# Optimization experiments

Measured on AMD Instinct MI355X. Metric: run time of the kernel, lower is better.

The kernel has to match this reference:

```python
import jax, jax.numpy as jnp
import numpy as np

H = 768
R = 24


def setup_inputs() -> dict:
    key = jax.random.key(0)
    ks = jax.random.split(key, 9)
    B, S = 4, 256
    hidden = jax.random.normal(ks[0], (B, S, H), dtype=jnp.float32)
    # ConcatHandshaking fc: Linear(2H -> H); torch weight shape (out,in)=(H,2H)
    fc_w = jax.random.normal(ks[1], (H, 2 * H), dtype=jnp.float32) * (1.0 / np.sqrt(2 * H))
    fc_b = jnp.zeros((H,), dtype=jnp.float32)
    # h2t: Linear(H -> 2)
    h2t_w = jax.random.normal(ks[2], (2, H), dtype=jnp.float32) * (1.0 / np.sqrt(H))
    h2t_b = jnp.zeros((2,), dtype=jnp.float32)
    # h2h / t2t TaggingProjector: R independent Linear(H -> 3), batched as (R,3,H)
    h2h_w = jax.random.normal(ks[3], (R, 3, H), dtype=jnp.float32) * (1.0 / np.sqrt(H))
    h2h_b = jnp.zeros((R, 3), dtype=jnp.float32)
    t2t_w = jax.random.normal(ks[4], (R, 3, H), dtype=jnp.float32) * (1.0 / np.sqrt(H))
    t2t_b = jnp.zeros((R, 3), dtype=jnp.float32)
    return {
        "hidden": hidden,
        "fc_w": fc_w, "fc_b": fc_b,
        "h2t_w": h2t_w, "h2t_b": h2t_b,
        "h2h_w": h2h_w, "h2h_b": h2h_b,
        "t2t_w": t2t_w, "t2t_b": t2t_b,
    }


def _handshaking(hidden, fc_w, fc_b):
    # hidden: (B, S, H). Pairs (i, j) with i <= j in row-major (torch loop) order.
    S = hidden.shape[1]
    idx_i, idx_j = jnp.triu_indices(S)  # each (P,), P = S(S+1)/2
    # concat([h_i, h_j]) @ W^T == h_i @ Wl^T + h_j @ Wr^T  (avoids (B,P,2H) buffer)
    Wl = fc_w[:, :H]  # (H, H)
    Wr = fc_w[:, H:]  # (H, H)
    left = jnp.einsum('bsh,oh->bso', hidden, Wl)   # (B, S, H)
    right = jnp.einsum('bsh,oh->bso', hidden, Wr)  # (B, S, H)
    hs = jnp.tanh(left[:, idx_i, :] + right[:, idx_j, :] + fc_b)  # (B, P, H)
    return hs


def reference(hidden, fc_w, fc_b, h2t_w, h2t_b, h2h_w, h2h_b, t2t_w, t2t_b):
    hs = _handshaking(hidden, fc_w, fc_b)  # (B, P, H)
    # h2t: plain Linear(H->2), logits (no softmax in original)
    h2t = jnp.einsum('bph,oh->bpo', hs, h2t_w) + h2t_b  # (B, P, 2)
    # TaggingProjector: batched per-relation Linear(H->3), then softmax over tags
    h2h = jax.nn.softmax(jnp.einsum('bph,rth->brpt', hs, h2h_w) + h2h_b[None, :, None, :], axis=-1)
    t2t = jax.nn.softmax(jnp.einsum('bph,rth->brpt', hs, t2t_w) + t2t_b[None, :, None, :], axis=-1)
    return (h2t, h2h, t2t)
```

## Files before the change

### kernel.cpp

```cpp
#include <hip/hip_runtime.h>
#include <hip/hip_bf16.h>

#define H 768
#define SEQ 256
#define NPAIR 32896
#define NTOT 131584
#define NOUTP 160
#define OFF_H2H 263168u
#define OFF_T2T 9737216u

#define N_BPK 122880
#define SCL 2.8853900817779268f

#define CH 32
#define NCH 24
#define BSLOT 12288
#define SLAB_STR 166

typedef short bf16x8 __attribute__((ext_vector_type(8)));
typedef float f32x4 __attribute__((ext_vector_type(4)));

__device__ __forceinline__ float bf_lo(int w){ return __uint_as_float(((unsigned)w) << 16); }
__device__ __forceinline__ float bf_hi(int w){ return __uint_as_float(((unsigned)w) & 0xffff0000u); }
__device__ __forceinline__ float bfu(unsigned short u){ return __uint_as_float(((unsigned)u) << 16); }
__device__ __forceinline__ int cvtpk(float lo, float hi) {
    int r;
    asm("v_cvt_pk_bf16_f32 %0, %1, %2" : "=v"(r) : "v"(lo), "v"(hi));
    return r;
}
__device__ __forceinline__ unsigned short bf16r(float x){
    unsigned int u = __float_as_uint(x);
    u += 0x7fffu + ((u >> 16) & 1u);
    return (unsigned short)(u >> 16);
}
__device__ __forceinline__ float tanh_e(float el, float er) {
    float e = el * er;
    return fmaf(-2.0f, __builtin_amdgcn_rcpf(e + 1.0f), 1.0f);
}
__device__ __forceinline__ bf16x8 prod_frag(int4 lv, int4 rv) {
    int4 st;
    st.x = cvtpk(tanh_e(bf_lo(lv.x), bf_lo(rv.x)), tanh_e(bf_hi(lv.x), bf_hi(rv.x)));
    st.y = cvtpk(tanh_e(bf_lo(lv.y), bf_lo(rv.y)), tanh_e(bf_hi(lv.y), bf_hi(rv.y)));
    st.z = cvtpk(tanh_e(bf_lo(lv.z), bf_lo(rv.z)), tanh_e(bf_hi(lv.z), bf_hi(rv.z)));
    st.w = cvtpk(tanh_e(bf_lo(lv.w), bf_lo(rv.w)), tanh_e(bf_hi(lv.w), bf_hi(rv.w)));
    return __builtin_bit_cast(bf16x8, st);
}

typedef const __attribute__((address_space(1))) unsigned int* as1_u32p;
typedef __attribute__((address_space(3))) unsigned int* as3_u32p;
__device__ __forceinline__ void gload_lds16(const void* g, void* l) {
    __builtin_amdgcn_global_load_lds((as1_u32p)g, (as3_u32p)l, 16, 0, 0);
}

__device__ __forceinline__ int row_start(int i) { return i * SEQ - (i * (i - 1)) / 2; }
__device__ __forceinline__ void pair_ij(int p, int& oi, int& oj) {
    double disc = 263169.0 - 8.0 * (double)p;
    int i = (int)((513.0 - sqrt(disc)) * 0.5);
    if (i > 0 && row_start(i) > p) --i;
    while (row_start(i + 1) <= p) ++i;
    oi = i;
    oj = i + (p - row_start(i));
}
__device__ __forceinline__ int batch_of(int g) {
    return (g >= 3 * NPAIR) ? 3 : (g >= 2 * NPAIR) ? 2 : (g >= NPAIR) ? 1 : 0;
}

__global__ __launch_bounds__(256) void pack_kernel(
    const float* __restrict__ h2t_w, const float* __restrict__ h2h_w,
    const float* __restrict__ t2t_w, const float* __restrict__ h2t_b,
    const float* __restrict__ h2h_b, const float* __restrict__ t2t_b,
    unsigned short* __restrict__ Bpk, float* __restrict__ bc)
{
    int idx = blockIdx.x * 256 + threadIdx.x;
    if (idx < N_BPK) {
        int j = idx & 7, lane = (idx >> 3) & 63, rest = idx >> 9;
        int f = rest % 10, c = rest / 10;
        int n = f * 16 + (lane & 15);
        int k = c * CH + ((lane >> 4) << 3) + j;
        float v = 0.f;
        if (n < 2)        v = h2t_w[n * H + k];
        else if (n < 74)  v = h2h_w[(n - 2) * H + k];
        else if (n < 146) v = t2t_w[(n - 74) * H + k];
        Bpk[c * 6144 + (idx - c * 5120)] = bf16r(v);
    } else if (idx < N_BPK + NOUTP) {
        int q = idx - N_BPK;
        float v = 0.f;
        if (q < 2)        v = h2t_b[q];
        else if (q < 74)  v = h2h_b[q - 2];
        else if (q < 146) v = t2t_b[q - 74];
        bc[q] = v;
    }
}

__global__ __launch_bounds__(256, 2) void lr_mfma(
    const float* __restrict__ hidden, const float* __restrict__ fc_w,
    const float* __restrict__ fc_b,
    unsigned short* __restrict__ LB, unsigned short* __restrict__ RB)
{
    __shared__ __align__(16) char sm[16384];
    const int tid = threadIdx.x, l = tid & 63, w = tid >> 6;
    const int wm = w >> 1, wn = w & 1;
    const int m0 = blockIdx.x * 64, n0 = blockIdx.y * 64;
    f32x4 acc[2][2] = {};
    for (int c = 0; c < 12; ++c) {
        const int k0 = c * 64;
        #pragma unroll
        for (int it = 0; it < 2; ++it) {
            int idx = tid + it * 256;
            int row = idx >> 3, k8 = idx & 7;
            const float4* src = reinterpret_cast<const float4*>(hidden + (size_t)(m0 + row) * H + k0 + k8 * 8);
            float4 a = src[0], bq = src[1];
            int4 st;
            st.x = cvtpk(a.x, a.y);  st.y = cvtpk(a.z, a.w);
            st.z = cvtpk(bq.x, bq.y); st.w = cvtpk(bq.z, bq.w);
            *reinterpret_cast<int4*>(sm + row * 128 + ((k8 * 16) ^ ((row & 7) << 4))) = st;
        }
        #pragma unroll
        for (int it = 0; it < 2; ++it) {
            int idx = tid + it * 256;
            int row = idx >> 3, k8 = idx & 7;
            const float* fsrc = (n0 < H)
                ? fc_w + (size_t)(n0 + row) * (2 * H) + k0 + k8 * 8
                : fc_w + (size_t)(n0 - H + row) * (2 * H) + H + k0 + k8 * 8;
            const float4* src = reinterpret_cast<const float4*>(fsrc);
            float4 a = src[0], bq = src[1];
            int4 st;
            st.x = cvtpk(a.x, a.y);  st.y = cvtpk(a.z, a.w);
            st.z = cvtpk(bq.x, bq.y); st.w = cvtpk(bq.z, bq.w);
            *reinterpret_cast<int4*>(sm + 8192 + row * 128 + ((k8 * 16) ^ ((row & 7) << 4))) = st;
        }
        __syncthreads();
        #pragma unroll
        for (int kk = 0; kk < 2; ++kk) {
            const int sl = kk * 4 + (l >> 4);
            const int swz = (l & 7) << 4;
            bf16x8 af[2], bfr[2];
            #pragma unroll
            for (int a = 0; a < 2; ++a) {
                int row = 32 * wm + 16 * a + (l & 15);
                af[a] = *reinterpret_cast<const bf16x8*>(sm + row * 128 + ((sl * 16) ^ swz));
            }
            #pragma unroll
            for (int f = 0; f < 2; ++f) {
                int row = 32 * wn + 16 * f + (l & 15);
                bfr[f] = *reinterpret_cast<const bf16x8*>(sm + 8192 + row * 128 + ((sl * 16) ^ swz));
            }
            #pragma unroll
            for (int a = 0; a < 2; ++a)
                #pragma unroll
                for (int f = 0; f < 2; ++f)
                    acc[a][f] = __builtin_amdgcn_mfma_f32_16x16x32_bf16(af[a], bfr[f], acc[a][f], 0, 0, 0);
        }
        __syncthreads();
    }
    #pragma unroll
    for (int a = 0; a < 2; ++a)
        #pragma unroll
        for (int f = 0; f < 2; ++f)
            #pragma unroll
            for (int r = 0; r < 4; ++r) {
                int row = m0 + 32 * wm + 16 * a + 4 * (l >> 4) + r;
                int col = n0 + 32 * wn + 16 * f + (l & 15);
                float v = acc[a][f][r];
                if (n0 < H) LB[(size_t)row * H + col] =
                    bf16r(__builtin_amdgcn_exp2f((v + fc_b[col]) * SCL));
                else        RB[(size_t)row * H + (col - H)] =
                    bf16r(__builtin_amdgcn_exp2f(v * SCL));
            }
}

__global__ __launch_bounds__(256, 4) void pair_mfma(
    const unsigned short* __restrict__ LB, const unsigned short* __restrict__ RB,
    const unsigned short* __restrict__ Bpk, const float* __restrict__ bc,
    float* __restrict__ out)
{
    __shared__ __align__(16) char sm[25216];
    int*   iOf  = reinterpret_cast<int*>(sm);
    int*   jOf  = reinterpret_cast<int*>(sm + 256);
    float* bc_s = reinterpret_cast<float*>(sm + 24576);

    const int tid = threadIdx.x, l = tid & 63, w = tid >> 6;
    const int g0 = blockIdx.x * 64;
    const int b = batch_of(g0);
    const int p0 = g0 - b * NPAIR;

    if (tid < 64) {
        int i, j; pair_ij(p0 + tid, i, j);
        iOf[tid] = (b * SEQ + i) * H;
        jOf[tid] = (b * SEQ + j) * H;
    }
    if (tid < NOUTP) bc_s[tid] = bc[tid];
    __syncthreads();

    const int row = 16 * w + (l & 15);
    const unsigned short* lp = LB + iOf[row] + ((l >> 4) << 3);
    const unsigned short* rp = RB + jOf[row] + ((l >> 4) << 3);
    __syncthreads();

    const char* bp = reinterpret_cast<const char*>(Bpk) + w * 1024 + l * 16;
    const int d0 = w * 1024;

    f32x4 acc[10] = {};
    int4 lv[3], rv[3];

    {
        gload_lds16(bp,        sm + d0);
        gload_lds16(bp + 4096, sm + 4096 + d0);
        gload_lds16(bp + 8192, sm + 8192 + d0);
        __builtin_amdgcn_sched_barrier(0);
    }
    lv[0] = *reinterpret_cast<const int4*>(lp);
    rv[0] = *reinterpret_cast<const int4*>(rp);
    lv[1] = *reinterpret_cast<const int4*>(lp + CH);
    rv[1] = *reinterpret_cast<const int4*>(rp + CH);
    asm volatile("s_waitcnt vmcnt(4)" ::: "memory");
    __builtin_amdgcn_s_barrier();
    __builtin_amdgcn_sched_barrier(0);

    #pragma unroll
    for (int c = 0; c < NCH - 2; ++c) {
        char* bufn = sm + (((c + 1) & 1) ? BSLOT : 0);
        const char* bn = bp + (c + 1) * BSLOT;
        gload_lds16(bn,        bufn + d0);
        gload_lds16(bn + 4096, bufn + 4096 + d0);
        gload_lds16(bn + 8192, bufn + 8192 + d0);
        __builtin_amdgcn_sched_barrier(0);
        bf16x8 a0 = prod_frag(lv[c % 3], rv[c % 3]);
        const int co = (c + 2) * CH;
        lv[(c + 2) % 3] = *reinterpret_cast<const int4*>(lp + co);
        rv[(c + 2) % 3] = *reinterpret_cast<const int4*>(rp + co);
        const char* bufc = sm + ((c & 1) ? BSLOT : 0);
        #pragma unroll
        for (int f = 0; f < 10; ++f) {
            bf16x8 bfr = *reinterpret_cast<const bf16x8*>(bufc + (f * 64 + l) * 16);
            acc[f] = __builtin_amdgcn_mfma_f32_16x16x32_bf16(a0, bfr, acc[f], 0, 0, 0);
        }
        asm volatile("s_waitcnt vmcnt(2)" ::: "memory");
        __builtin_amdgcn_s_barrier();
        __builtin_amdgcn_sched_barrier(0);
    }
    {
        char* bufn = sm + BSLOT;
        const char* bn = bp + 23 * BSLOT;
        gload_lds16(bn,        bufn + d0);
        gload_lds16(bn + 4096, bufn + 4096 + d0);
        gload_lds16(bn + 8192, bufn + 8192 + d0);
        __builtin_amdgcn_sched_barrier(0);
        bf16x8 a0 = prod_frag(lv[22 % 3], rv[22 % 3]);
        const char* bufc = sm;
        #pragma unroll
        for (int f = 0; f < 10; ++f) {
            bf16x8 bfr = *reinterpret_cast<const bf16x8*>(bufc + (f * 64 + l) * 16);
            acc[f] = __builtin_amdgcn_mfma_f32_16x16x32_bf16(a0, bfr, acc[f], 0, 0, 0);
        }
        asm volatile("s_waitcnt vmcnt(0)" ::: "memory");
        __builtin_amdgcn_s_barrier();
        __builtin_amdgcn_sched_barrier(0);
    }
    {
        bf16x8 a0 = prod_frag(lv[23 % 3], rv[23 % 3]);
        const char* bufc = sm + BSLOT;
        #pragma unroll
        for (int f = 0; f < 10; ++f) {
            bf16x8 bfr = *reinterpret_cast<const bf16x8*>(bufc + (f * 64 + l) * 16);
            acc[f] = __builtin_amdgcn_mfma_f32_16x16x32_bf16(a0, bfr, acc[f], 0, 0, 0);
        }
    }
    asm volatile("s_waitcnt lgkmcnt(0)" ::: "memory");
    __builtin_amdgcn_s_barrier();

    unsigned short* slab = reinterpret_cast<unsigned short*>(sm);
    #pragma unroll
    for (int f = 0; f < 10; ++f)
        #pragma unroll
        for (int r = 0; r < 4; ++r) {
            int rw = 16 * w + 4 * (l >> 4) + r;
            slab[rw * SLAB_STR + f * 16 + (l & 15)] = bf16r(acc[f][r]);
        }
    __syncthreads();

    if (tid < 128) {
        int pr = tid >> 1, tt = tid & 1;
        float val = bfu(slab[pr * SLAB_STR + tt]) + bc_s[tt];
        __builtin_nontemporal_store(val, &out[(size_t)(g0 + pr) * 2 + tt]);
    }
    #pragma unroll
    for (int it = 0; it < 12; ++it) {
        int item = it * 256 + tid;
        int pr = item & 63, rr = item >> 6;
        int p = p0 + pr;
        int ob = 2 + rr * 3;
        const unsigned short* sp = slab + pr * SLAB_STR + ob;
        float l0 = bfu(sp[0]) + bc_s[ob + 0];
        float l1 = bfu(sp[1]) + bc_s[ob + 1];
        float l2 = bfu(sp[2]) + bc_s[ob + 2];
        float mx = fmaxf(l0, fmaxf(l1, l2));
        float e0 = __expf(l0 - mx), e1 = __expf(l1 - mx), e2 = __expf(l2 - mx);
        float inv = __fdividef(1.0f, e0 + e1 + e2);
        size_t base = (rr < 24)
            ? (size_t)OFF_H2H + ((size_t)(b * 24 + rr) * NPAIR + p) * 3
            : (size_t)OFF_T2T + ((size_t)(b * 24 + rr - 24) * NPAIR + p) * 3;
        __builtin_nontemporal_store(e0 * inv, &out[base + 0]);
        __builtin_nontemporal_store(e1 * inv, &out[base + 1]);
        __builtin_nontemporal_store(e2 * inv, &out[base + 2]);
    }
}

extern "C" void kernel_launch(void* const* d_in, const int* in_sizes, int n_in,
                              void* d_out, int out_size, void* d_ws, size_t ws_size,
                              hipStream_t stream) {
    const float* hidden = (const float*)d_in[0];
    const float* fc_w   = (const float*)d_in[1];
    const float* fc_b   = (const float*)d_in[2];
    const float* h2t_w  = (const float*)d_in[3];
    const float* h2t_b  = (const float*)d_in[4];
    const float* h2h_w  = (const float*)d_in[5];
    const float* h2h_b  = (const float*)d_in[6];
    const float* t2t_w  = (const float*)d_in[7];
    const float* t2t_b  = (const float*)d_in[8];

    char* wsb = (char*)d_ws;
    unsigned short* LBw  = (unsigned short*)(wsb);
    unsigned short* RBw  = (unsigned short*)(wsb + 1572864);
    unsigned short* Bpk  = (unsigned short*)(wsb + 3145728);
    float*          bc   = (float*)        (wsb + 3440640);

    float* out = (float*)d_out;

    pack_kernel<<<(N_BPK + NOUTP + 255) / 256, 256, 0, stream>>>(
        h2t_w, h2h_w, t2t_w, h2t_b, h2h_b, t2t_b, Bpk, bc);
    lr_mfma<<<dim3(16, 24), 256, 0, stream>>>(hidden, fc_w, fc_b, LBw, RBw);
    pair_mfma<<<NTOT / 64, 256, 0, stream>>>(LBw, RBw, Bpk, bc, out);
}
```

Before: 89.30 us.

## Merge pack and LR kernels; triple-buffer Bpk LDS pipeline with setprio

Folds the weight-packing kernel and the left/right projection GEMM into one launch, using block-index ranges to pick the role. This removes a kernel launch and the serialization between them. In the pair kernel, the B-fragment LDS ring goes from double to triple buffering, prefetching two chunks ahead with relaxed vmcnt waits. s_setprio is raised around the MFMA bursts. The triple buffer raises LDS use from about 25 KB to 37.5 KB per block, which may reduce occupancy at 4 blocks per CU.

```diff
diff --git a/kernel.cpp b/kernel.cpp
--- a/kernel.cpp
+++ b/kernel.cpp
@@ -16,6 +16,9 @@
 #define NCH 24
 #define BSLOT 12288
 #define SLAB_STR 166
+
+#define PACK_BLOCKS 481
+#define LR_BLOCKS 384
 
 typedef short bf16x8 __attribute__((ext_vector_type(8)));
 typedef float f32x4 __attribute__((ext_vector_type(4)));
@@ -65,42 +68,43 @@
     return (g >= 3 * NPAIR) ? 3 : (g >= 2 * NPAIR) ? 2 : (g >= NPAIR) ? 1 : 0;
 }
 
-__global__ __launch_bounds__(256) void pack_kernel(
+__global__ __launch_bounds__(256, 2) void setup_kernel(
+    const float* __restrict__ hidden, const float* __restrict__ fc_w,
+    const float* __restrict__ fc_b,
     const float* __restrict__ h2t_w, const float* __restrict__ h2h_w,
     const float* __restrict__ t2t_w, const float* __restrict__ h2t_b,
     const float* __restrict__ h2h_b, const float* __restrict__ t2t_b,
-    unsigned short* __restrict__ Bpk, float* __restrict__ bc)
-{
-    int idx = blockIdx.x * 256 + threadIdx.x;
-    if (idx < N_BPK) {
-        int j = idx & 7, lane = (idx >> 3) & 63, rest = idx >> 9;
-        int f = rest % 10, c = rest / 10;
-        int n = f * 16 + (lane & 15);
-        int k = c * CH + ((lane >> 4) << 3) + j;
-        float v = 0.f;
-        if (n < 2)        v = h2t_w[n * H + k];
-        else if (n < 74)  v = h2h_w[(n - 2) * H + k];
-        else if (n < 146) v = t2t_w[(n - 74) * H + k];
-        Bpk[c * 6144 + (idx - c * 5120)] = bf16r(v);
-    } else if (idx < N_BPK + NOUTP) {
-        int q = idx - N_BPK;
-        float v = 0.f;
-        if (q < 2)        v = h2t_b[q];
-        else if (q < 74)  v = h2h_b[q - 2];
-        else if (q < 146) v = t2t_b[q - 74];
-        bc[q] = v;
-    }
-}
-
-__global__ __launch_bounds__(256, 2) void lr_mfma(
-    const float* __restrict__ hidden, const float* __restrict__ fc_w,
-    const float* __restrict__ fc_b,
+    unsigned short* __restrict__ Bpk, float* __restrict__ bc,
     unsigned short* __restrict__ LB, unsigned short* __restrict__ RB)
 {
+    const int tid = threadIdx.x;
+    if (blockIdx.x < PACK_BLOCKS) {
+        int idx = blockIdx.x * 256 + tid;
+        if (idx < N_BPK) {
+            int j = idx & 7, lane = (idx >> 3) & 63, rest = idx >> 9;
+            int f = rest % 10, c = rest / 10;
+            int n = f * 16 + (lane & 15);
+            int k = c * CH + ((lane >> 4) << 3) + j;
+            float v = 0.f;
+            if (n < 2)        v = h2t_w[n * H + k];
+            else if (n < 74)  v = h2h_w[(n - 2) * H + k];
+            else if (n < 146) v = t2t_w[(n - 74) * H + k];
+            Bpk[c * 6144 + (idx - c * 5120)] = bf16r(v);
+        } else if (idx < N_BPK + NOUTP) {
+            int q = idx - N_BPK;
+            float v = 0.f;
+            if (q < 2)        v = h2t_b[q];
+            else if (q < 74)  v = h2h_b[q - 2];
+            else if (q < 146) v = t2t_b[q - 74];
+            bc[q] = v;
+        }
+        return;
+    }
     __shared__ __align__(16) char sm[16384];
-    const int tid = threadIdx.x, l = tid & 63, w = tid >> 6;
+    const int q = blockIdx.x - PACK_BLOCKS;
+    const int m0 = (q & 15) * 64, n0 = (q >> 4) * 64;
+    const int l = tid & 63, w = tid >> 6;
     const int wm = w >> 1, wn = w & 1;
-    const int m0 = blockIdx.x * 64, n0 = blockIdx.y * 64;
     f32x4 acc[2][2] = {};
     for (int c = 0; c < 12; ++c) {
         const int k0 = c * 64;
@@ -174,10 +178,10 @@
     const unsigned short* __restrict__ Bpk, const float* __restrict__ bc,
     float* __restrict__ out)
 {
-    __shared__ __align__(16) char sm[25216];
+    __shared__ __align__(16) char sm[37504];
     int*   iOf  = reinterpret_cast<int*>(sm);
     int*   jOf  = reinterpret_cast<int*>(sm + 256);
-    float* bc_s = reinterpret_cast<float*>(sm + 24576);
+    float* bc_s = reinterpret_cast<float*>(sm + 36864);
 
     const int tid = threadIdx.x, l = tid & 63, w = tid >> 6;
     const int g0 = blockIdx.x * 64;
@@ -208,19 +212,23 @@
         gload_lds16(bp + 4096, sm + 4096 + d0);
         gload_lds16(bp + 8192, sm + 8192 + d0);
         __builtin_amdgcn_sched_barrier(0);
-    }
-    lv[0] = *reinterpret_cast<const int4*>(lp);
-    rv[0] = *reinterpret_cast<const int4*>(rp);
-    lv[1] = *reinterpret_cast<const int4*>(lp + CH);
-    rv[1] = *reinterpret_cast<const int4*>(rp + CH);
-    asm volatile("s_waitcnt vmcnt(4)" ::: "memory");
-    __builtin_amdgcn_s_barrier();
-    __builtin_amdgcn_sched_barrier(0);
+        lv[0] = *reinterpret_cast<const int4*>(lp);
+        rv[0] = *reinterpret_cast<const int4*>(rp);
+        gload_lds16(bp + BSLOT,        sm + BSLOT + d0);
+        gload_lds16(bp + BSLOT + 4096, sm + BSLOT + 4096 + d0);
+        gload_lds16(bp + BSLOT + 8192, sm + BSLOT + 8192 + d0);
+        __builtin_amdgcn_sched_barrier(0);
+        lv[1] = *reinterpret_cast<const int4*>(lp + CH);
+        rv[1] = *reinterpret_cast<const int4*>(rp + CH);
+        asm volatile("s_waitcnt vmcnt(7)" ::: "memory");
+        __builtin_amdgcn_s_barrier();
+        __builtin_amdgcn_sched_barrier(0);
+    }
 
     #pragma unroll
     for (int c = 0; c < NCH - 2; ++c) {
-        char* bufn = sm + (((c + 1) & 1) ? BSLOT : 0);
-        const char* bn = bp + (c + 1) * BSLOT;
+        char* bufn = sm + ((c + 2) % 3) * BSLOT;
+        const char* bn = bp + (c + 2) * BSLOT;
         gload_lds16(bn,        bufn + d0);
         gload_lds16(bn + 4096, bufn + 4096 + d0);
         gload_lds16(bn + 8192, bufn + 8192 + d0);
@@ -229,37 +237,35 @@
         const int co = (c + 2) * CH;
         lv[(c + 2) % 3] = *reinterpret_cast<const int4*>(lp + co);
         rv[(c + 2) % 3] = *reinterpret_cast<const int4*>(rp + co);
-        const char* bufc = sm + ((c & 1) ? BSLOT : 0);
+        const char* bufc = sm + (c % 3) * BSLOT;
+        __builtin_amdgcn_s_setprio(1);
         #pragma unroll
         for (int f = 0; f < 10; ++f) {
             bf16x8 bfr = *reinterpret_cast<const bf16x8*>(bufc + (f * 64 + l) * 16);
             acc[f] = __builtin_amdgcn_mfma_f32_16x16x32_bf16(a0, bfr, acc[f], 0, 0, 0);
         }
-        asm volatile("s_waitcnt vmcnt(2)" ::: "memory");
+        __builtin_amdgcn_s_setprio(0);
+        asm volatile("s_waitcnt vmcnt(5)" ::: "memory");
         __builtin_amdgcn_s_barrier();
         __builtin_amdgcn_sched_barrier(0);
     }
     {
-        char* bufn = sm + BSLOT;
-        const char* bn = bp + 23 * BSLOT;
-        gload_lds16(bn,        bufn + d0);
-        gload_lds16(bn + 4096, bufn + 4096 + d0);
-        gload_lds16(bn + 8192, bufn + 8192 + d0);
-        __builtin_amdgcn_sched_barrier(0);
         bf16x8 a0 = prod_frag(lv[22 % 3], rv[22 % 3]);
-        const char* bufc = sm;
+        const char* bufc = sm + (22 % 3) * BSLOT;
+        __builtin_amdgcn_s_setprio(1);
         #pragma unroll
         for (int f = 0; f < 10; ++f) {
             bf16x8 bfr = *reinterpret_cast<const bf16x8*>(bufc + (f * 64 + l) * 16);
             acc[f] = __builtin_amdgcn_mfma_f32_16x16x32_bf16(a0, bfr, acc[f], 0, 0, 0);
         }
+        __builtin_amdgcn_s_setprio(0);
         asm volatile("s_waitcnt vmcnt(0)" ::: "memory");
         __builtin_amdgcn_s_barrier();
         __builtin_amdgcn_sched_barrier(0);
     }
     {
         bf16x8 a0 = prod_frag(lv[23 % 3], rv[23 % 3]);
-        const char* bufc = sm + BSLOT;
+        const char* bufc = sm + (23 % 3) * BSLOT;
         #pragma unroll
         for (int f = 0; f < 10; ++f) {
             bf16x8 bfr = *reinterpret_cast<const bf16x8*>(bufc + (f * 64 + l) * 16);
@@ -327,8 +333,8 @@
 
     float* out = (float*)d_out;
 
-    pack_kernel<<<(N_BPK + NOUTP + 255) / 256, 256, 0, stream>>>(
-        h2t_w, h2h_w, t2t_w, h2t_b, h2h_b, t2t_b, Bpk, bc);
-    lr_mfma<<<dim3(16, 24), 256, 0, stream>>>(hidden, fc_w, fc_b, LBw, RBw);
+    setup_kernel<<<PACK_BLOCKS + LR_BLOCKS, 256, 0, stream>>>(
+        hidden, fc_w, fc_b, h2t_w, h2h_w, t2t_w, h2t_b, h2h_b, t2t_b,
+        Bpk, bc, LBw, RBw);
     pair_mfma<<<NTOT / 64, 256, 0, stream>>>(LBw, RBw, Bpk, bc, out);
 }
```

After: 86.16 us. 3.5% less time.
